# Kernel optimization log

Hardware: AMD Instinct MI355X
Metric: run time of the kernel (lower is better)

The kernel has to match this reference:

```python
import jax, jax.numpy as jnp
import numpy as np

H = 64  # GRU hidden size (out_channels)

def _gru_layer(xs, W_ih, W_hh, b_ih, b_hh):
    # xs: [T, B, I]; W_ih: [3H, I]; W_hh: [3H, H]; gate order r,z,n (PyTorch)
    x_proj = jnp.einsum('tbi,gi->tbg', xs, W_ih) + b_ih  # [T, B, 3H], precomputed
    def step(h, xp):
        gh = h @ W_hh.T + b_hh                 # [B, 3H]
        ir, iz, inn = jnp.split(xp, 3, axis=-1)
        hr, hz, hn = jnp.split(gh, 3, axis=-1)
        r = jax.nn.sigmoid(ir + hr)
        z = jax.nn.sigmoid(iz + hz)
        n = jnp.tanh(inn + r * hn)
        h_new = (1.0 - z) * n + z * h
        return h_new, h_new
    h0 = jnp.zeros((xs.shape[1], H), xs.dtype)
    _, ys = jax.lax.scan(step, h0, x_proj)
    return ys  # [T, B, H]

def setup_inputs() -> dict:
    key = jax.random.key(0)
    ks = jax.random.split(key, 13)
    B, C, T = 1024, 64, 512
    s = 1.0 / np.sqrt(H)
    u = lambda k, shape: jax.random.uniform(k, shape, jnp.float32, -s, s)
    return {
        'x': jax.random.normal(ks[0], (B, C, T), jnp.float32),
        'W_ih0': u(ks[1], (3 * H, C)),  'W_hh0': u(ks[2], (3 * H, H)),
        'b_ih0': u(ks[3], (3 * H,)),    'b_hh0': u(ks[4], (3 * H,)),
        'W_ih1': u(ks[5], (3 * H, H)),  'W_hh1': u(ks[6], (3 * H, H)),
        'b_ih1': u(ks[7], (3 * H,)),    'b_hh1': u(ks[8], (3 * H,)),
        'W1': u(ks[9], (32, H)),  'b1': u(ks[10], (32,)),
        'W2': u(ks[11], (4, 32)), 'b2': u(ks[12], (4,)),
    }

def reference(x, W_ih0, W_hh0, b_ih0, b_hh0, W_ih1, W_hh1, b_ih1, b_hh1, W1, b1, W2, b2):
    xs = jnp.transpose(x, (2, 0, 1))                      # [T, B, C]
    h1 = _gru_layer(xs, W_ih0, W_hh0, b_ih0, b_hh0)       # [T, B, H]
    h2 = _gru_layer(h1, W_ih1, W_hh1, b_ih1, b_hh1)       # [T, B, H]
    h_last = h2[-1]                                       # [B, H] == permute(1,2,0)[:,:,-1]
    y = jax.nn.relu(h_last @ W1.T + b1) @ W2.T + b2       # [B, nclasses]
    return y
```

## Files before the change

### kernel.cpp

```cpp
#include <hip/hip_runtime.h>

#define T_STEPS 512
#define HID 64

typedef short bf16x8 __attribute__((ext_vector_type(8)));
typedef float f32x4 __attribute__((ext_vector_type(4)));

__device__ __forceinline__ float sigm(float x) {
  return __builtin_amdgcn_rcpf(1.f + __expf(-x));
}
__device__ __forceinline__ float tanh_fast(float x) {
  return 1.f - 2.f * __builtin_amdgcn_rcpf(__expf(2.f * x) + 1.f);
}

__device__ __forceinline__ void split1(float v, short* hi, short* lo) {
  unsigned u = __float_as_uint(v);
  float r = v - __uint_as_float(u & 0xffff0000u);
  *hi = (short)(u >> 16);
  *lo = (short)(__float_as_uint(r) >> 16);
}

__device__ __forceinline__ void split8(const float* __restrict__ p, bf16x8& hi, bf16x8& lo) {
  float v[8];
  *(float4*)&v[0] = *(const float4*)p;
  *(float4*)&v[4] = *(const float4*)(p + 4);
  #pragma unroll
  for (int i = 0; i < 8; ++i) {
    unsigned u = __float_as_uint(v[i]);
    float r = v[i] - __uint_as_float(u & 0xffff0000u);
    hi[i] = (short)(u >> 16);
    lo[i] = (short)(__float_as_uint(r) >> 16);
  }
}

#define MM(acc, A, B) acc = __builtin_amdgcn_mfma_f32_16x16x32_bf16((A), (B), (acc), 0, 0, 0)

#define GP4(acc, V0, V1, NM) do { \
    MM(acc, V0, NM##h0); MM(acc, V1, NM##h1); \
    MM(acc, V0, NM##l0); MM(acc, V1, NM##l1); } while (0)

#define WFRAG(NM, Wp, goff) \
  bf16x8 NM##h0, NM##l0, NM##h1, NM##l1; \
  split8((Wp) + (goff) * (64 * HID) + wrowoff, NM##h0, NM##l0); \
  split8((Wp) + (goff) * (64 * HID) + wrowoff + 32, NM##h1, NM##l1)

__global__ __launch_bounds__(512, 2) void gru_mfma(
    const float* __restrict__ x,
    const float* __restrict__ Wih0, const float* __restrict__ Whh0,
    const float* __restrict__ bih0, const float* __restrict__ bhh0,
    const float* __restrict__ Wih1, const float* __restrict__ Whh1,
    const float* __restrict__ bih1, const float* __restrict__ bhh1,
    const float* __restrict__ W1, const float* __restrict__ b1,
    const float* __restrict__ W2, const float* __restrict__ b2,
    float* __restrict__ out)
{
  const int tid   = threadIdx.x;
  const int lane  = tid & 63;
  const int wv    = tid >> 6;
  const int wq    = wv & 3;
  const int layer = wv >> 2;
  const int nloc  = lane & 15;
  const int quad  = lane >> 4;
  const int b0    = blockIdx.x << 2;

  __shared__ __align__(16) short xs[2][1024];
  __shared__ __align__(16) short hA[2][1024];
  __shared__ __align__(16) short hB[2][1024];
  __shared__ float hfin[256];
  __shared__ float msf[128];

  const float* Wih  = layer ? Wih1 : Wih0;
  const float* Whh  = layer ? Whh1 : Whh0;
  const float* bihp = layer ? bih1 : bih0;
  const float* bhhp = layer ? bhh1 : bhh0;

  const int wrowoff = (16 * wq + nloc) * HID + 8 * quad;
  WFRAG(ir, Wih, 0); WFRAG(iz, Wih, 1); WFRAG(in, Wih, 2);
  WFRAG(hr, Whh, 0); WFRAG(hz, Whh, 1); WFRAG(hn, Whh, 2);

  const int jg = 16 * wq + nloc;
  const float b_r = bihp[jg] + bhhp[jg];
  const float b_z = bihp[jg + 64] + bhhp[jg + 64];
  const float b_i = bihp[jg + 128], b_h = bhhp[jg + 128];

  const int ra0 = nloc * 64 + (((quad    ) ^ (nloc & 7)) << 3);
  const int ra1 = nloc * 64 + (((quad + 4) ^ (nloc & 7)) << 3);
  const int hwrH = quad * 256 +      (((jg >> 3) ^ ( (quad & 1) << 2)     ) << 3) + (jg & 7);
  const int hwrL = quad * 256 + 64 + (((jg >> 3) ^ (((quad & 1) << 2) | 1)) << 3) + (jg & 7);
  const int xwrH = wq * 256 +      (((lane >> 3) ^ ( (wq & 1) << 2)     ) << 3) + (lane & 7);
  const int xwrL = wq * 256 + 64 + (((lane >> 3) ^ (((wq & 1) << 2) | 1)) << 3) + (lane & 7);

  short* Hown = layer ? &hB[0][0] : &hA[0][0];
  short* Vin  = layer ? &hA[0][0] : &xs[0][0];

  const float* xptr = x + ((size_t)(b0 + wq) * HID + lane) * T_STEPS;

  for (int i = tid; i < 2048; i += 512) {
    ((short*)xs)[i] = 0; ((short*)hA)[i] = 0; ((short*)hB)[i] = 0;
  }
  __syncthreads();
  if (!layer) { short h, l; split1(xptr[0], &h, &l); xs[1][xwrH] = h; xs[1][xwrL] = l; }
  __syncthreads();

  float hp = 0.f;

  #define STEP_BODY(RB, WB, F0, TT) do { \
    bf16x8 H0 = *(const bf16x8*)&Hown[(RB) + ra0], H1 = *(const bf16x8*)&Hown[(RB) + ra1]; \
    bf16x8 V0 = *(const bf16x8*)&Vin[(RB) + ra0],  V1 = *(const bf16x8*)&Vin[(RB) + ra1]; \
    float xn = 0.f; \
    if (!layer) xn = xptr[((TT) + 1) & (T_STEPS - 1)]; \
    f32x4 sRh = {b_r, 0.f, 0.f, 0.f}, sRx = {0.f, 0.f, 0.f, 0.f}; \
    f32x4 sZh = {b_z, 0.f, 0.f, 0.f}, sZx = {0.f, 0.f, 0.f, 0.f}; \
    f32x4 sHh = {b_h, 0.f, 0.f, 0.f}, sIx = {b_i, 0.f, 0.f, 0.f}; \
    __builtin_amdgcn_s_setprio(1); \
    GP4(sRh, H0, H1, hr); GP4(sRx, V0, V1, ir); \
    GP4(sZh, H0, H1, hz); GP4(sZx, V0, V1, iz); \
    float rr = sigm((sRx[0] + sRx[1]) + (sRh[0] + sRh[1])); \
    float zz = sigm((sZx[0] + sZx[1]) + (sZh[0] + sZh[1])); \
    GP4(sHh, H0, H1, hn); GP4(sIx, V0, V1, in); \
    __builtin_amdgcn_s_setprio(0); \
    float n = tanh_fast((sIx[0] + sIx[1]) + rr * (sHh[0] + sHh[1])); \
    float hnew = n + zz * (hp - n); \
    hp = ((F0) && layer && (TT) == 0) ? 0.f : hnew; \
    { short h, l; split1(hp, &h, &l); Hown[(WB) + hwrH] = h; Hown[(WB) + hwrL] = l; } \
    if (!layer) { short h, l; split1(xn, &h, &l); \
                  ((short*)xs)[(WB) + xwrH] = h; ((short*)xs)[(WB) + xwrL] = l; } \
    __syncthreads(); \
  } while (0)

  #pragma unroll 1
  for (int t = 0; t < T_STEPS; t += 2) {
    STEP_BODY(1024, 0, 1, t);
    STEP_BODY(0, 1024, 0, t + 1);
  }
  #undef STEP_BODY

  if (layer) {
    const f32x4 z4 = {0.f, 0.f, 0.f, 0.f};
    const int rb = 1 << 10;
    bf16x8 H0 = *(const bf16x8*)&Hown[rb + ra0], H1 = *(const bf16x8*)&Hown[rb + ra1];
    bf16x8 V0 = *(const bf16x8*)&Vin[rb + ra0],  V1 = *(const bf16x8*)&Vin[rb + ra1];
    f32x4 sRh = z4, sZh = z4, sHh = z4, sRx = z4, sZx = z4, sIx = z4;
    GP4(sRh, H0, H1, hr);
    GP4(sRx, V0, V1, ir);
    GP4(sZh, H0, H1, hz);
    GP4(sZx, V0, V1, iz);
    GP4(sHh, H0, H1, hn);
    GP4(sIx, V0, V1, in);
    float r  = sigm((sRx[0] + sRx[1]) + (sRh[0] + sRh[1]) + b_r);
    float zz = sigm((sZx[0] + sZx[1]) + (sZh[0] + sZh[1]) + b_z);
    float n  = tanh_fast(((sIx[0] + sIx[1]) + b_i) + r * ((sHh[0] + sHh[1]) + b_h));
    hp = n + zz * (hp - n);
    hfin[quad * 64 + jg] = hp;
  }
  __syncthreads();

  if (tid < 128) {
    const int bb = tid >> 5, u = tid & 31;
    float acc = b1[u];
    const float* w1r = W1 + u * HID;
    #pragma unroll
    for (int k = 0; k < 64; ++k)
      acc = fmaf(w1r[k], hfin[bb * 64 + k], acc);
    msf[(bb << 5) + u] = fmaxf(acc, 0.f);
  }
  __syncthreads();
  if (tid < 16) {
    const int bb = tid >> 2, c = tid & 3;
    float acc = b2[c];
    const float* w2r = W2 + (c << 5);
    #pragma unroll
    for (int u = 0; u < 32; ++u)
      acc = fmaf(w2r[u], msf[(bb << 5) + u], acc);
    out[(size_t)(b0 + bb) * 4 + c] = acc;
  }
}

extern "C" void kernel_launch(void* const* d_in, const int* in_sizes, int n_in,
                              void* d_out, int out_size, void* d_ws, size_t ws_size,
                              hipStream_t stream) {
  const float* x    = (const float*)d_in[0];
  const float* Wih0 = (const float*)d_in[1];
  const float* Whh0 = (const float*)d_in[2];
  const float* bih0 = (const float*)d_in[3];
  const float* bhh0 = (const float*)d_in[4];
  const float* Wih1 = (const float*)d_in[5];
  const float* Whh1 = (const float*)d_in[6];
  const float* bih1 = (const float*)d_in[7];
  const float* bhh1 = (const float*)d_in[8];
  const float* W1   = (const float*)d_in[9];
  const float* b1   = (const float*)d_in[10];
  const float* W2   = (const float*)d_in[11];
  const float* b2   = (const float*)d_in[12];
  float* out = (float*)d_out;

  hipLaunchKernelGGL(gru_mfma, dim3(256), dim3(512), 0, stream,
                     x, Wih0, Whh0, bih0, bhh0, Wih1, Whh1, bih1, bhh1,
                     W1, b1, W2, b2, out);
}
```

Baseline: 442.7 us.

## Pack hidden state and layer input into one shared A-tile per layer

Puts the recurrent hidden state and the layer input into a single 16-row LDS operand tile per layer. Rows 0-1 hold h (hi/lo) and rows 2-3 hold the input (hi/lo), so each step issues two LDS fragment reads instead of four. Layer 0 now writes its hidden state twice, once into its own tile and once into layer 1's input rows. The input-gate sums are read from accumulator rows 2-3 instead of a separate accumulator. This removes an LDS buffer and half the per-step fragment loads, at the cost of an extra duplicate store in layer 0.

After: 450.4 us. No clear change (+1.7%).

```diff
diff --git a/kernel.cpp b/kernel.cpp
--- a/kernel.cpp
+++ b/kernel.cpp
@@ -63,9 +63,8 @@
   const int quad  = lane >> 4;
   const int b0    = blockIdx.x << 2;
 
-  __shared__ __align__(16) short xs[2][1024];
-  __shared__ __align__(16) short hA[2][1024];
-  __shared__ __align__(16) short hB[2][1024];
+  __shared__ __align__(16) short aL0[2][1024];
+  __shared__ __align__(16) short aL1[2][1024];
   __shared__ float hfin[256];
   __shared__ float msf[128];
 
@@ -85,46 +84,49 @@
 
   const int ra0 = nloc * 64 + (((quad    ) ^ (nloc & 7)) << 3);
   const int ra1 = nloc * 64 + (((quad + 4) ^ (nloc & 7)) << 3);
-  const int hwrH = quad * 256 +      (((jg >> 3) ^ ( (quad & 1) << 2)     ) << 3) + (jg & 7);
-  const int hwrL = quad * 256 + 64 + (((jg >> 3) ^ (((quad & 1) << 2) | 1)) << 3) + (jg & 7);
-  const int xwrH = wq * 256 +      (((lane >> 3) ^ ( (wq & 1) << 2)     ) << 3) + (lane & 7);
-  const int xwrL = wq * 256 + 64 + (((lane >> 3) ^ (((wq & 1) << 2) | 1)) << 3) + (lane & 7);
-
-  short* Hown = layer ? &hB[0][0] : &hA[0][0];
-  short* Vin  = layer ? &hA[0][0] : &xs[0][0];
+  const int hwrH  = quad * 256 +       (((jg >> 3) ^ ( (quad & 1) << 2)       ) << 3) + (jg & 7);
+  const int hwrL  = quad * 256 +  64 + (((jg >> 3) ^ (((quad & 1) << 2) | 1)) << 3) + (jg & 7);
+  const int hwr2H = quad * 256 + 128 + (((jg >> 3) ^ (((quad & 1) << 2) | 2)) << 3) + (jg & 7);
+  const int hwr2L = quad * 256 + 192 + (((jg >> 3) ^ (((quad & 1) << 2) | 3)) << 3) + (jg & 7);
+  const int xwrH  = wq * 256 + 128 + (((lane >> 3) ^ (((wq & 1) << 2) | 2)) << 3) + (lane & 7);
+  const int xwrL  = wq * 256 + 192 + (((lane >> 3) ^ (((wq & 1) << 2) | 3)) << 3) + (lane & 7);
+
+  short* Ar      = layer ? &aL1[0][0] : &aL0[0][0];
+  short* aL1flat = &aL1[0][0];
+  short* aL0flat = &aL0[0][0];
 
   const float* xptr = x + ((size_t)(b0 + wq) * HID + lane) * T_STEPS;
 
-  for (int i = tid; i < 2048; i += 512) {
-    ((short*)xs)[i] = 0; ((short*)hA)[i] = 0; ((short*)hB)[i] = 0;
-  }
-  __syncthreads();
-  if (!layer) { short h, l; split1(xptr[0], &h, &l); xs[1][xwrH] = h; xs[1][xwrL] = l; }
+  for (int i = tid; i < 2048; i += 512) { aL0flat[i] = 0; aL1flat[i] = 0; }
+  __syncthreads();
+  if (!layer) { short h, l; split1(xptr[0], &h, &l);
+                aL0flat[1024 + xwrH] = h; aL0flat[1024 + xwrL] = l; }
   __syncthreads();
 
   float hp = 0.f;
 
   #define STEP_BODY(RB, WB, F0, TT) do { \
-    bf16x8 H0 = *(const bf16x8*)&Hown[(RB) + ra0], H1 = *(const bf16x8*)&Hown[(RB) + ra1]; \
-    bf16x8 V0 = *(const bf16x8*)&Vin[(RB) + ra0],  V1 = *(const bf16x8*)&Vin[(RB) + ra1]; \
+    bf16x8 HV0 = *(const bf16x8*)&Ar[(RB) + ra0], HV1 = *(const bf16x8*)&Ar[(RB) + ra1]; \
     float xn = 0.f; \
     if (!layer) xn = xptr[((TT) + 1) & (T_STEPS - 1)]; \
     f32x4 sRh = {b_r, 0.f, 0.f, 0.f}, sRx = {0.f, 0.f, 0.f, 0.f}; \
     f32x4 sZh = {b_z, 0.f, 0.f, 0.f}, sZx = {0.f, 0.f, 0.f, 0.f}; \
-    f32x4 sHh = {b_h, 0.f, 0.f, 0.f}, sIx = {b_i, 0.f, 0.f, 0.f}; \
+    f32x4 sHh = {b_h, 0.f, 0.f, 0.f}, sIx = {0.f, 0.f, b_i, 0.f}; \
     __builtin_amdgcn_s_setprio(1); \
-    GP4(sRh, H0, H1, hr); GP4(sRx, V0, V1, ir); \
-    GP4(sZh, H0, H1, hz); GP4(sZx, V0, V1, iz); \
-    float rr = sigm((sRx[0] + sRx[1]) + (sRh[0] + sRh[1])); \
-    float zz = sigm((sZx[0] + sZx[1]) + (sZh[0] + sZh[1])); \
-    GP4(sHh, H0, H1, hn); GP4(sIx, V0, V1, in); \
+    GP4(sRh, HV0, HV1, hr); GP4(sRx, HV0, HV1, ir); \
+    GP4(sZh, HV0, HV1, hz); GP4(sZx, HV0, HV1, iz); \
+    float rr = sigm((sRx[2] + sRx[3]) + (sRh[0] + sRh[1])); \
+    float zz = sigm((sZx[2] + sZx[3]) + (sZh[0] + sZh[1])); \
+    GP4(sHh, HV0, HV1, hn); GP4(sIx, HV0, HV1, in); \
     __builtin_amdgcn_s_setprio(0); \
-    float n = tanh_fast((sIx[0] + sIx[1]) + rr * (sHh[0] + sHh[1])); \
+    float n = tanh_fast((sIx[2] + sIx[3]) + rr * (sHh[0] + sHh[1])); \
     float hnew = n + zz * (hp - n); \
     hp = ((F0) && layer && (TT) == 0) ? 0.f : hnew; \
-    { short h, l; split1(hp, &h, &l); Hown[(WB) + hwrH] = h; Hown[(WB) + hwrL] = l; } \
+    { short h, l; split1(hp, &h, &l); \
+      Ar[(WB) + hwrH] = h; Ar[(WB) + hwrL] = l; \
+      if (!layer) { aL1flat[(WB) + hwr2H] = h; aL1flat[(WB) + hwr2L] = l; } } \
     if (!layer) { short h, l; split1(xn, &h, &l); \
-                  ((short*)xs)[(WB) + xwrH] = h; ((short*)xs)[(WB) + xwrL] = l; } \
+                  aL0flat[(WB) + xwrH] = h; aL0flat[(WB) + xwrL] = l; } \
     __syncthreads(); \
   } while (0)
 
@@ -137,19 +139,17 @@
 
   if (layer) {
     const f32x4 z4 = {0.f, 0.f, 0.f, 0.f};
-    const int rb = 1 << 10;
-    bf16x8 H0 = *(const bf16x8*)&Hown[rb + ra0], H1 = *(const bf16x8*)&Hown[rb + ra1];
-    bf16x8 V0 = *(const bf16x8*)&Vin[rb + ra0],  V1 = *(const bf16x8*)&Vin[rb + ra1];
+    bf16x8 HV0 = *(const bf16x8*)&Ar[1024 + ra0], HV1 = *(const bf16x8*)&Ar[1024 + ra1];
     f32x4 sRh = z4, sZh = z4, sHh = z4, sRx = z4, sZx = z4, sIx = z4;
-    GP4(sRh, H0, H1, hr);
-    GP4(sRx, V0, V1, ir);
-    GP4(sZh, H0, H1, hz);
-    GP4(sZx, V0, V1, iz);
-    GP4(sHh, H0, H1, hn);
-    GP4(sIx, V0, V1, in);
-    float r  = sigm((sRx[0] + sRx[1]) + (sRh[0] + sRh[1]) + b_r);
-    float zz = sigm((sZx[0] + sZx[1]) + (sZh[0] + sZh[1]) + b_z);
-    float n  = tanh_fast(((sIx[0] + sIx[1]) + b_i) + r * ((sHh[0] + sHh[1]) + b_h));
+    GP4(sRh, HV0, HV1, hr);
+    GP4(sRx, HV0, HV1, ir);
+    GP4(sZh, HV0, HV1, hz);
+    GP4(sZx, HV0, HV1, iz);
+    GP4(sHh, HV0, HV1, hn);
+    GP4(sIx, HV0, HV1, in);
+    float r  = sigm((sRx[2] + sRx[3]) + (sRh[0] + sRh[1]) + b_r);
+    float zz = sigm((sZx[2] + sZx[3]) + (sZh[0] + sZh[1]) + b_z);
+    float n  = tanh_fast(((sIx[2] + sIx[3]) + b_i) + r * ((sHh[0] + sHh[1]) + b_h));
     hp = n + zz * (hp - n);
     hfin[quad * 64 + jg] = hp;
   }
```
